# Optimization experiments

Hardware: AMD Instinct MI355X
Metric: run time of the kernel (lower is better)

The kernel has to match this reference:

```python
import jax, jax.numpy as jnp
import numpy as np

N_NODES = 50000
N_EDGES = 640000
D = 128
L = 3


def setup_inputs() -> dict:
    key = jax.random.key(0)
    k1, k2, k3, k4 = jax.random.split(key, 4)
    x = jax.random.normal(k1, (N_NODES, D), dtype=jnp.float32)
    # Glorot-ish scale so activations stay O(1) across 3 layers
    Ws = jax.random.normal(k2, (L, D, D), dtype=jnp.float32) * (1.0 / np.sqrt(D))
    bs = jnp.zeros((L, D), dtype=jnp.float32)
    edge_src = jax.random.randint(k3, (N_EDGES,), 0, N_NODES, dtype=jnp.int32)
    edge_dst = jax.random.randint(k4, (N_EDGES,), 0, N_NODES, dtype=jnp.int32)
    return {"x": x, "Ws": Ws, "bs": bs, "edge_src": edge_src, "edge_dst": edge_dst}


def reference(x, Ws, bs, edge_src, edge_dst):
    n = x.shape[0]
    ones = jnp.ones(edge_src.shape[0], dtype=x.dtype)
    # degrees, clamped to 1 as in dgl GraphConv(norm='both')
    deg_out = jnp.maximum(jax.ops.segment_sum(ones, edge_src, num_segments=n), 1.0)
    deg_in = jnp.maximum(jax.ops.segment_sum(ones, edge_dst, num_segments=n), 1.0)
    inv_sqrt_out = jax.lax.rsqrt(deg_out)[:, None]  # [N,1]
    inv_sqrt_in = jax.lax.rsqrt(deg_in)[:, None]    # [N,1]
    for l in range(Ws.shape[0]):
        h = x * inv_sqrt_out                         # src normalization
        msg = h[edge_src]                            # [E,D] gather
        agg = jax.ops.segment_sum(msg, edge_dst, num_segments=n)  # [N,D] scatter-add
        h = agg * inv_sqrt_in                        # dst normalization
        x = jax.nn.relu(h @ Ws[l] + bs[l])           # linear + ReLU
    return x
```

## Files before the change

kernel.cpp:

```cpp
#include <hip/hip_runtime.h>
#include <hip/hip_fp16.h>

typedef __attribute__((ext_vector_type(8))) _Float16 half8;
typedef __attribute__((ext_vector_type(4))) float f32x4;
typedef unsigned int u32;
typedef unsigned short u16;

#define ELL_PAD 64
#define NCHUNK 64
#define RSZ 8192


__global__ __launch_bounds__(256) void hist2(const int* __restrict__ esrc,
                                             const int* __restrict__ edst,
                                             u32* __restrict__ psrc,
                                             u32* __restrict__ pdst,
                                             const float* __restrict__ Ws,
                                             _Float16* __restrict__ Whi,
                                             _Float16* __restrict__ Wlo,
                                             int E, int N, int chunk, int R,
                                             int histBlocks, int packTotal) {
  __shared__ u32 bs_[RSZ];
  __shared__ u32 bd_[RSZ];
  if (blockIdx.x >= histBlocks) {
    int i = (blockIdx.x - histBlocks) * 256 + threadIdx.x;
    if (i < packTotal) {
      int lane  = i & 63;
      int kstep = (i >> 6) & 3;
      int ntile = (i >> 8) & 7;
      int layer = i >> 11;
      int n  = ntile * 16 + (lane & 15);
      int k0 = kstep * 32 + (lane >> 4) * 8;
      const float* W = Ws + (size_t)layer * 128 * 128;
      size_t base = (size_t)i * 8;
      for (int j = 0; j < 8; j++) {
        float v = W[(k0 + j) * 128 + n];
        _Float16 hi = (_Float16)v;
        Whi[base + j] = hi;
        Wlo[base + j] = (_Float16)(v - (float)hi);
      }
    }
    return;
  }
  int c = blockIdx.x / R;
  int r = blockIdx.x % R;
  int base = r * RSZ;
  int hi = min(RSZ, N - base);
  if (hi <= 0) return;
  for (int j = threadIdx.x; j < RSZ; j += 256) { bs_[j] = 0; bd_[j] = 0; }
  __syncthreads();
  int e0 = c * chunk;
  int e1 = min(E, e0 + chunk);
  for (int i = e0 + threadIdx.x; i < e1; i += 256) {
    unsigned ls = (unsigned)(esrc[i] - base);
    unsigned ld = (unsigned)(edst[i] - base);
    if (ls < (unsigned)RSZ) atomicAdd(&bs_[ls], 1u);
    if (ld < (unsigned)RSZ) atomicAdd(&bd_[ld], 1u);
  }
  __syncthreads();
  u32* ds = psrc + (size_t)c * N + base;
  u32* dd = pdst + (size_t)c * N + base;
  for (int j = threadIdx.x; j < hi; j += 256) { ds[j] = bs_[j]; dd[j] = bd_[j]; }
}


__global__ __launch_bounds__(256) void prep(const u32* __restrict__ psrc,
                                            u32* __restrict__ pdst,
                                            int* __restrict__ deg_out,
                                            int* __restrict__ deg_in, int N) {
  int i = blockIdx.x * 256 + threadIdx.x;
  if (i >= N) return;
  u32 s0 = 0, s1 = 0, s2 = 0, s3 = 0;
#pragma unroll
  for (int c = 0; c < NCHUNK; c += 4) {
    s0 += psrc[(size_t)(c + 0) * N + i];
    s1 += psrc[(size_t)(c + 1) * N + i];
    s2 += psrc[(size_t)(c + 2) * N + i];
    s3 += psrc[(size_t)(c + 3) * N + i];
  }
  deg_out[i] = (int)(s0 + s1 + s2 + s3);
  u32 cnt[NCHUNK];
#pragma unroll
  for (int c = 0; c < NCHUNK; c++) cnt[c] = pdst[(size_t)c * N + i];
  u32 run = (u32)i * ELL_PAD;
#pragma unroll
  for (int c = 0; c < NCHUNK; c++) { u32 t = cnt[c]; cnt[c] = run; run += t; }
#pragma unroll
  for (int c = 0; c < NCHUNK; c++) pdst[(size_t)c * N + i] = cnt[c];
  deg_in[i] = (int)(run - (u32)i * ELL_PAD);
}


__global__ __launch_bounds__(256) void xscale(const float* __restrict__ x,
                                              const int* __restrict__ deg_out,
                                              __half2* __restrict__ xh, int n64) {
  int gid = blockIdx.x * 256 + threadIdx.x;
  if (gid >= n64) return;
  int row = gid >> 6;
  int d = deg_out[row]; if (d < 1) d = 1;
  float s = rsqrtf((float)d);
  float2 v = ((const float2*)x)[gid];
  xh[gid] = __floats2half2_rn(v.x * s, v.y * s);
}


__global__ __launch_bounds__(256) void place(const int* __restrict__ esrc,
                                             const int* __restrict__ edst,
                                             const u32* __restrict__ pdst,
                                             u16* __restrict__ ell,
                                             int E, int N, int chunk, int R) {
  __shared__ u32 cur[RSZ];
  int c = blockIdx.x / R;
  int r = blockIdx.x % R;
  int base = r * RSZ;
  int hi = min(RSZ, N - base);
  if (hi <= 0) return;
  for (int j = threadIdx.x; j < hi; j += 256)
    cur[j] = pdst[(size_t)c * N + base + j];
  __syncthreads();
  int e0 = c * chunk;
  int e1 = min(E, e0 + chunk);
  for (int i = e0 + threadIdx.x; i < e1; i += 256) {
    int d = edst[i];
    unsigned loc = (unsigned)(d - base);
    if (loc < (unsigned)hi) {
      u32 p = atomicAdd(&cur[loc], 1u);
      u32 idx = p - (u32)d * ELL_PAD;
      if (idx < ELL_PAD) ell[p] = (u16)esrc[i];
    }
  }
}


__global__ __launch_bounds__(512) void layer16(const __half2* __restrict__ xh,
                                               const int* __restrict__ deg_in,
                                               const u16* __restrict__ ell,
                                               const _Float16* __restrict__ Whi,
                                               const _Float16* __restrict__ Wlo,
                                               const float* __restrict__ bias,
                                               const int* __restrict__ deg_out,
                                               __half* __restrict__ out16,
                                               float* __restrict__ out32, int n) {
  __shared__ _Float16 As[16 * 136];
  const int wave = threadIdx.x >> 6;
  const int lane = threadIdx.x & 63;
  const int rowBase = blockIdx.x * 16;

  {
    int r0 = rowBase + wave * 2, r1 = r0 + 1;
    int d0 = (r0 < n) ? deg_in[r0] : 0;
    int d1 = (r1 < n) ? deg_in[r1] : 0;
    int l0 = d0 > ELL_PAD ? ELL_PAD : d0;
    int l1 = d1 > ELL_PAD ? ELL_PAD : d1;
    const u16* ep0 = ell + (size_t)(r0 < n ? r0 : 0) * ELL_PAD;
    const u16* ep1 = ell + (size_t)(r1 < n ? r1 : 0) * ELL_PAD;
    float ax0 = 0.f, ay0 = 0.f, ax1 = 0.f, ay1 = 0.f;

    int m = (l0 < l1 ? l0 : l1) & ~3;
    int e = 0;
    for (; e < m; e += 4) {
      ushort4 ia = *(const ushort4*)&ep0[e];
      ushort4 ib = *(const ushort4*)&ep1[e];
      __half2 a0 = xh[(size_t)ia.x * 64 + lane];
      __half2 a1 = xh[(size_t)ia.y * 64 + lane];
      __half2 a2 = xh[(size_t)ia.z * 64 + lane];
      __half2 a3 = xh[(size_t)ia.w * 64 + lane];
      __half2 b0 = xh[(size_t)ib.x * 64 + lane];
      __half2 b1 = xh[(size_t)ib.y * 64 + lane];
      __half2 b2 = xh[(size_t)ib.z * 64 + lane];
      __half2 b3 = xh[(size_t)ib.w * 64 + lane];
      float2 u0 = __half22float2(a0), u1 = __half22float2(a1);
      float2 u2 = __half22float2(a2), u3 = __half22float2(a3);
      float2 w0 = __half22float2(b0), w1 = __half22float2(b1);
      float2 w2 = __half22float2(b2), w3 = __half22float2(b3);
      ax0 += (u0.x + u1.x) + (u2.x + u3.x);
      ay0 += (u0.y + u1.y) + (u2.y + u3.y);
      ax1 += (w0.x + w1.x) + (w2.x + w3.x);
      ay1 += (w0.y + w1.y) + (w2.y + w3.y);
    }
    int e0i = e;
    for (; e0i + 4 <= l0; e0i += 4) {
      ushort4 ia = *(const ushort4*)&ep0[e0i];
      __half2 a0 = xh[(size_t)ia.x * 64 + lane];
      __half2 a1 = xh[(size_t)ia.y * 64 + lane];
      __half2 a2 = xh[(size_t)ia.z * 64 + lane];
      __half2 a3 = xh[(size_t)ia.w * 64 + lane];
      float2 u0 = __half22float2(a0), u1 = __half22float2(a1);
      float2 u2 = __half22float2(a2), u3 = __half22float2(a3);
      ax0 += (u0.x + u1.x) + (u2.x + u3.x);
      ay0 += (u0.y + u1.y) + (u2.y + u3.y);
    }
    for (; e0i < l0; e0i++) {
      float2 v = __half22float2(xh[(size_t)ep0[e0i] * 64 + lane]);
      ax0 += v.x; ay0 += v.y;
    }
    int e1i = e;
    for (; e1i + 4 <= l1; e1i += 4) {
      ushort4 ib = *(const ushort4*)&ep1[e1i];
      __half2 b0 = xh[(size_t)ib.x * 64 + lane];
      __half2 b1 = xh[(size_t)ib.y * 64 + lane];
      __half2 b2 = xh[(size_t)ib.z * 64 + lane];
      __half2 b3 = xh[(size_t)ib.w * 64 + lane];
      float2 w0 = __half22float2(b0), w1 = __half22float2(b1);
      float2 w2 = __half22float2(b2), w3 = __half22float2(b3);
      ax1 += (w0.x + w1.x) + (w2.x + w3.x);
      ay1 += (w0.y + w1.y) + (w2.y + w3.y);
    }
    for (; e1i < l1; e1i++) {
      float2 v = __half22float2(xh[(size_t)ep1[e1i] * 64 + lane]);
      ax1 += v.x; ay1 += v.y;
    }

    float si0 = rsqrtf((float)(d0 < 1 ? 1 : d0));
    float si1 = rsqrtf((float)(d1 < 1 ? 1 : d1));
    *(__half2*)&As[(size_t)(wave * 2 + 0) * 136 + lane * 2] =
        __floats2half2_rn(ax0 * si0, ay0 * si0);
    *(__half2*)&As[(size_t)(wave * 2 + 1) * 136 + lane * 2] =
        __floats2half2_rn(ax1 * si1, ay1 * si1);
  }
  __syncthreads();

  const int quad = lane >> 4;
  const int l16  = lane & 15;
  f32x4 acc = (f32x4){0.f, 0.f, 0.f, 0.f};
#pragma unroll
  for (int ks = 0; ks < 4; ks++) {
    half8 a = *(const half8*)&As[(size_t)l16 * 136 + ks * 32 + quad * 8];
    half8 bh = *(const half8*)&Whi[((wave * 4 + ks) * 64 + lane) * 8];
    half8 bl = *(const half8*)&Wlo[((wave * 4 + ks) * 64 + lane) * 8];
    acc = __builtin_amdgcn_mfma_f32_16x16x32_f16(a, bh, acc, 0, 0, 0);
    acc = __builtin_amdgcn_mfma_f32_16x16x32_f16(a, bl, acc, 0, 0, 0);
  }

  const int r0 = rowBase + quad * 4;
  const int col = wave * 16 + l16;
  const float bv = bias[col];
#pragma unroll
  for (int r = 0; r < 4; r++) {
    int row = r0 + r;
    if (row < n) {
      float v = fmaxf(acc[r] + bv, 0.f);
      if (out16) {
        int d = deg_out[row]; if (d < 1) d = 1;
        out16[(size_t)row * 128 + col] = __float2half(v * rsqrtf((float)d));
      } else {
        out32[(size_t)row * 128 + col] = v;
      }
    }
  }
}


extern "C" void kernel_launch(void* const* d_in, const int* in_sizes, int n_in,
                              void* d_out, int out_size, void* d_ws, size_t ws_size,
                              hipStream_t stream) {
  const float* x   = (const float*)d_in[0];
  const float* Ws  = (const float*)d_in[1];
  const float* bs  = (const float*)d_in[2];
  const int* esrc  = (const int*)d_in[3];
  const int* edst  = (const int*)d_in[4];

  const int D = 128;
  const int N = in_sizes[0] / D;
  const int E = in_sizes[3];
  const int L = in_sizes[1] / (D * D);
  const int Npad = ((N + 15) / 16) * 16;
  const int chunk = (E + NCHUNK - 1) / NCHUNK;
  const int R = (N + RSZ - 1) / RSZ;
  const int histBlocks = NCHUNK * R;
  const int packTotal = L * 2048;
  const int packBlocks = (packTotal + 255) / 256;

  char* base = (char*)d_ws;
  size_t off = 0;
  auto alloc = [&](size_t bytes) {
    char* p = base + off;
    off = (off + bytes + 255) & ~(size_t)255;
    return p;
  };
  int*      deg_out = (int*)alloc((size_t)N * 4);
  int*      deg_in  = (int*)alloc((size_t)N * 4);
  u16*      ell     = (u16*)alloc((size_t)N * ELL_PAD * 2);
  _Float16* Whi     = (_Float16*)alloc((size_t)L * 16384 * 2);
  _Float16* Wlo     = (_Float16*)alloc((size_t)L * 16384 * 2);
  _Float16* xh0     = (_Float16*)alloc((size_t)Npad * 128 * 2);
  _Float16* xh1     = (_Float16*)alloc((size_t)Npad * 128 * 2);
  u32*      psrc    = (u32*)alloc((size_t)NCHUNK * N * 4);
  u32*      pdst    = (u32*)alloc((size_t)NCHUNK * N * 4);

  hist2<<<dim3(histBlocks + packBlocks), dim3(256), 0, stream>>>(
      esrc, edst, psrc, pdst, Ws, Whi, Wlo, E, N, chunk, R, histBlocks, packTotal);
  prep<<<dim3((N + 255) / 256), dim3(256), 0, stream>>>(psrc, pdst, deg_out, deg_in, N);
  xscale<<<dim3((N * 64 + 255) / 256), dim3(256), 0, stream>>>(
      x, deg_out, (__half2*)xh0, N * 64);
  place<<<dim3(histBlocks), dim3(256), 0, stream>>>(
      esrc, edst, pdst, ell, E, N, chunk, R);

  float* outf = (float*)d_out;
  _Float16* ping[2] = {xh0, xh1};
  const dim3 lgrid(Npad / 16), lblk(512);

  for (int l = 0; l < L; l++) {
    bool last = (l == L - 1);
    layer16<<<lgrid, lblk, 0, stream>>>(
        (const __half2*)ping[l & 1], deg_in, ell,
        Whi + (size_t)l * 16384, Wlo + (size_t)l * 16384,
        bs + (size_t)l * D, deg_out,
        last ? nullptr : (__half*)ping[(l + 1) & 1],
        last ? outf : nullptr, N);
  }
}
```

Before: 264.1 us.

## Build ELL with global atomics and gather four neighbors per wave with 16-byte loads

The chunked shared-memory histogram, prefix-scan and placement kernels are replaced by one edge-parallel kernel. It uses global atomics on the degree arrays to count degrees and place ELL entries directly, which drops the large per-chunk partial-count buffers and two launches. ELL rows are padded to a multiple of four with a dummy zero-filled node, so the aggregation loop needs no scalar tails. Each wave now splits into four 16-lane groups that each gather a different neighbor row with half8 loads, then combine the partial sums with cross-lane shuffles. In exchange, neighbor order within each ELL row becomes nondeterministic and the global atomics contend on high-degree nodes.

Result: no change. 262.6 us (-0.6%).

```diff
diff --git a/kernel.cpp b/kernel.cpp
--- a/kernel.cpp
+++ b/kernel.cpp
@@ -5,95 +5,69 @@
 typedef __attribute__((ext_vector_type(4))) float f32x4;
 typedef unsigned int u32;
 typedef unsigned short u16;
+typedef unsigned long long u64;
 
 #define ELL_PAD 64
-#define NCHUNK 64
-#define RSZ 8192
-
-
-__global__ __launch_bounds__(256) void hist2(const int* __restrict__ esrc,
+
+
+__global__ __launch_bounds__(256) void initpack(int* __restrict__ deg_out,
+                                                int* __restrict__ deg_in,
+                                                u32* __restrict__ xz0,
+                                                u32* __restrict__ xz1,
+                                                const float* __restrict__ Ws,
+                                                _Float16* __restrict__ Whi,
+                                                _Float16* __restrict__ Wlo,
+                                                int N, int padU32, int zb, int packTotal) {
+  int b = blockIdx.x;
+  if (b < zb) {
+    int i = b * 256 + threadIdx.x;
+    if (i < N) { deg_out[i] = 0; deg_in[i] = 0; }
+    if (b == 0) {
+      for (int j = threadIdx.x; j < padU32; j += 256) { xz0[j] = 0; xz1[j] = 0; }
+    }
+    return;
+  }
+  int i = (b - zb) * 256 + threadIdx.x;
+  if (i < packTotal) {
+    int lane  = i & 63;
+    int kstep = (i >> 6) & 3;
+    int ntile = (i >> 8) & 7;
+    int layer = i >> 11;
+    int nn = ntile * 16 + (lane & 15);
+    int k0 = kstep * 32 + (lane >> 4) * 8;
+    const float* W = Ws + (size_t)layer * 128 * 128;
+    size_t base = (size_t)i * 8;
+    for (int j = 0; j < 8; j++) {
+      float v = W[(k0 + j) * 128 + nn];
+      _Float16 hi = (_Float16)v;
+      Whi[base + j] = hi;
+      Wlo[base + j] = (_Float16)(v - (float)hi);
+    }
+  }
+}
+
+
+__global__ __launch_bounds__(256) void build(const int* __restrict__ esrc,
                                              const int* __restrict__ edst,
-                                             u32* __restrict__ psrc,
-                                             u32* __restrict__ pdst,
-                                             const float* __restrict__ Ws,
-                                             _Float16* __restrict__ Whi,
-                                             _Float16* __restrict__ Wlo,
-                                             int E, int N, int chunk, int R,
-                                             int histBlocks, int packTotal) {
-  __shared__ u32 bs_[RSZ];
-  __shared__ u32 bd_[RSZ];
-  if (blockIdx.x >= histBlocks) {
-    int i = (blockIdx.x - histBlocks) * 256 + threadIdx.x;
-    if (i < packTotal) {
-      int lane  = i & 63;
-      int kstep = (i >> 6) & 3;
-      int ntile = (i >> 8) & 7;
-      int layer = i >> 11;
-      int n  = ntile * 16 + (lane & 15);
-      int k0 = kstep * 32 + (lane >> 4) * 8;
-      const float* W = Ws + (size_t)layer * 128 * 128;
-      size_t base = (size_t)i * 8;
-      for (int j = 0; j < 8; j++) {
-        float v = W[(k0 + j) * 128 + n];
-        _Float16 hi = (_Float16)v;
-        Whi[base + j] = hi;
-        Wlo[base + j] = (_Float16)(v - (float)hi);
-      }
-    }
-    return;
-  }
-  int c = blockIdx.x / R;
-  int r = blockIdx.x % R;
-  int base = r * RSZ;
-  int hi = min(RSZ, N - base);
-  if (hi <= 0) return;
-  for (int j = threadIdx.x; j < RSZ; j += 256) { bs_[j] = 0; bd_[j] = 0; }
-  __syncthreads();
-  int e0 = c * chunk;
-  int e1 = min(E, e0 + chunk);
-  for (int i = e0 + threadIdx.x; i < e1; i += 256) {
-    unsigned ls = (unsigned)(esrc[i] - base);
-    unsigned ld = (unsigned)(edst[i] - base);
-    if (ls < (unsigned)RSZ) atomicAdd(&bs_[ls], 1u);
-    if (ld < (unsigned)RSZ) atomicAdd(&bd_[ld], 1u);
-  }
-  __syncthreads();
-  u32* ds = psrc + (size_t)c * N + base;
-  u32* dd = pdst + (size_t)c * N + base;
-  for (int j = threadIdx.x; j < hi; j += 256) { ds[j] = bs_[j]; dd[j] = bd_[j]; }
-}
-
-
-__global__ __launch_bounds__(256) void prep(const u32* __restrict__ psrc,
-                                            u32* __restrict__ pdst,
-                                            int* __restrict__ deg_out,
-                                            int* __restrict__ deg_in, int N) {
+                                             int* __restrict__ deg_out,
+                                             int* __restrict__ deg_in,
+                                             u16* __restrict__ ell, int E) {
   int i = blockIdx.x * 256 + threadIdx.x;
-  if (i >= N) return;
-  u32 s0 = 0, s1 = 0, s2 = 0, s3 = 0;
-#pragma unroll
-  for (int c = 0; c < NCHUNK; c += 4) {
-    s0 += psrc[(size_t)(c + 0) * N + i];
-    s1 += psrc[(size_t)(c + 1) * N + i];
-    s2 += psrc[(size_t)(c + 2) * N + i];
-    s3 += psrc[(size_t)(c + 3) * N + i];
-  }
-  deg_out[i] = (int)(s0 + s1 + s2 + s3);
-  u32 cnt[NCHUNK];
-#pragma unroll
-  for (int c = 0; c < NCHUNK; c++) cnt[c] = pdst[(size_t)c * N + i];
-  u32 run = (u32)i * ELL_PAD;
-#pragma unroll
-  for (int c = 0; c < NCHUNK; c++) { u32 t = cnt[c]; cnt[c] = run; run += t; }
-#pragma unroll
-  for (int c = 0; c < NCHUNK; c++) pdst[(size_t)c * N + i] = cnt[c];
-  deg_in[i] = (int)(run - (u32)i * ELL_PAD);
+  if (i >= E) return;
+  int s = esrc[i];
+  int d = edst[i];
+  atomicAdd(&deg_out[s], 1);
+  int p = atomicAdd(&deg_in[d], 1);
+  if (p < ELL_PAD) ell[(u32)d * ELL_PAD + (u32)p] = (u16)s;
 }
 
 
 __global__ __launch_bounds__(256) void xscale(const float* __restrict__ x,
                                               const int* __restrict__ deg_out,
-                                              __half2* __restrict__ xh, int n64) {
+                                              const int* __restrict__ deg_in,
+                                              __half2* __restrict__ xh,
+                                              u16* __restrict__ ell,
+                                              int N, int n64) {
   int gid = blockIdx.x * 256 + threadIdx.x;
   if (gid >= n64) return;
   int row = gid >> 6;
@@ -101,38 +75,17 @@
   float s = rsqrtf((float)d);
   float2 v = ((const float2*)x)[gid];
   xh[gid] = __floats2half2_rn(v.x * s, v.y * s);
-}
-
-
-__global__ __launch_bounds__(256) void place(const int* __restrict__ esrc,
-                                             const int* __restrict__ edst,
-                                             const u32* __restrict__ pdst,
-                                             u16* __restrict__ ell,
-                                             int E, int N, int chunk, int R) {
-  __shared__ u32 cur[RSZ];
-  int c = blockIdx.x / R;
-  int r = blockIdx.x % R;
-  int base = r * RSZ;
-  int hi = min(RSZ, N - base);
-  if (hi <= 0) return;
-  for (int j = threadIdx.x; j < hi; j += 256)
-    cur[j] = pdst[(size_t)c * N + base + j];
-  __syncthreads();
-  int e0 = c * chunk;
-  int e1 = min(E, e0 + chunk);
-  for (int i = e0 + threadIdx.x; i < e1; i += 256) {
-    int d = edst[i];
-    unsigned loc = (unsigned)(d - base);
-    if (loc < (unsigned)hi) {
-      u32 p = atomicAdd(&cur[loc], 1u);
-      u32 idx = p - (u32)d * ELL_PAD;
-      if (idx < ELL_PAD) ell[p] = (u16)esrc[i];
-    }
-  }
-}
-
-
-__global__ __launch_bounds__(512) void layer16(const __half2* __restrict__ xh,
+  if ((gid & 63) == 0) {
+    int c = deg_in[row];
+    int l = c > ELL_PAD ? ELL_PAD : c;
+    int t = (l + 3) & ~3;
+    u16* ep = ell + (u32)row * ELL_PAD;
+    for (int q = l; q < t; q++) ep[q] = (u16)N;
+  }
+}
+
+
+__global__ __launch_bounds__(512) void layer16(const _Float16* __restrict__ xh,
                                                const int* __restrict__ deg_in,
                                                const u16* __restrict__ ell,
                                                const _Float16* __restrict__ Whi,
@@ -144,7 +97,12 @@
   __shared__ _Float16 As[16 * 136];
   const int wave = threadIdx.x >> 6;
   const int lane = threadIdx.x & 63;
+  const int sub  = lane & 15;
+  const int grp  = lane >> 4;
+  const int sh   = grp << 4;
+  const u32 sub16 = (u32)sub * 16u;
   const int rowBase = blockIdx.x * 16;
+  const char* __restrict__ xb = (const char*)xh;
 
   {
     int r0 = rowBase + wave * 2, r1 = r0 + 1;
@@ -152,92 +110,99 @@
     int d1 = (r1 < n) ? deg_in[r1] : 0;
     int l0 = d0 > ELL_PAD ? ELL_PAD : d0;
     int l1 = d1 > ELL_PAD ? ELL_PAD : d1;
-    const u16* ep0 = ell + (size_t)(r0 < n ? r0 : 0) * ELL_PAD;
-    const u16* ep1 = ell + (size_t)(r1 < n ? r1 : 0) * ELL_PAD;
-    float ax0 = 0.f, ay0 = 0.f, ax1 = 0.f, ay1 = 0.f;
-
-    int m = (l0 < l1 ? l0 : l1) & ~3;
+    int t0 = (l0 + 3) & ~3;
+    int t1 = (l1 + 3) & ~3;
+    const u16* ep0 = ell + (u32)(r0 < n ? r0 : 0) * ELL_PAD;
+    const u16* ep1 = ell + (u32)(r1 < n ? r1 : 0) * ELL_PAD;
+
+    float a0[8] = {0.f, 0.f, 0.f, 0.f, 0.f, 0.f, 0.f, 0.f};
+    float a1[8] = {0.f, 0.f, 0.f, 0.f, 0.f, 0.f, 0.f, 0.f};
+
+    int m = t0 < t1 ? t0 : t1;
     int e = 0;
+    for (; e + 8 <= m; e += 8) {
+      u64 wa0 = *(const u64*)&ep0[e];
+      u64 wa1 = *(const u64*)&ep0[e + 4];
+      u64 wb0 = *(const u64*)&ep1[e];
+      u64 wb1 = *(const u64*)&ep1[e + 4];
+      u32 ia0 = ((u32)(wa0 >> sh) & 0xFFFFu) * 256u + sub16;
+      u32 ia1 = ((u32)(wa1 >> sh) & 0xFFFFu) * 256u + sub16;
+      u32 ib0 = ((u32)(wb0 >> sh) & 0xFFFFu) * 256u + sub16;
+      u32 ib1 = ((u32)(wb1 >> sh) & 0xFFFFu) * 256u + sub16;
+      half8 va0 = *(const half8*)(xb + ia0);
+      half8 va1 = *(const half8*)(xb + ia1);
+      half8 vb0 = *(const half8*)(xb + ib0);
+      half8 vb1 = *(const half8*)(xb + ib1);
+#pragma unroll
+      for (int j = 0; j < 8; j++) {
+        a0[j] += (float)va0[j] + (float)va1[j];
+        a1[j] += (float)vb0[j] + (float)vb1[j];
+      }
+    }
     for (; e < m; e += 4) {
-      ushort4 ia = *(const ushort4*)&ep0[e];
-      ushort4 ib = *(const ushort4*)&ep1[e];
-      __half2 a0 = xh[(size_t)ia.x * 64 + lane];
-      __half2 a1 = xh[(size_t)ia.y * 64 + lane];
-      __half2 a2 = xh[(size_t)ia.z * 64 + lane];
-      __half2 a3 = xh[(size_t)ia.w * 64 + lane];
-      __half2 b0 = xh[(size_t)ib.x * 64 + lane];
-      __half2 b1 = xh[(size_t)ib.y * 64 + lane];
-      __half2 b2 = xh[(size_t)ib.z * 64 + lane];
-      __half2 b3 = xh[(size_t)ib.w * 64 + lane];
-      float2 u0 = __half22float2(a0), u1 = __half22float2(a1);
-      float2 u2 = __half22float2(a2), u3 = __half22float2(a3);
-      float2 w0 = __half22float2(b0), w1 = __half22float2(b1);
-      float2 w2 = __half22float2(b2), w3 = __half22float2(b3);
-      ax0 += (u0.x + u1.x) + (u2.x + u3.x);
-      ay0 += (u0.y + u1.y) + (u2.y + u3.y);
-      ax1 += (w0.x + w1.x) + (w2.x + w3.x);
-      ay1 += (w0.y + w1.y) + (w2.y + w3.y);
-    }
-    int e0i = e;
-    for (; e0i + 4 <= l0; e0i += 4) {
-      ushort4 ia = *(const ushort4*)&ep0[e0i];
-      __half2 a0 = xh[(size_t)ia.x * 64 + lane];
-      __half2 a1 = xh[(size_t)ia.y * 64 + lane];
-      __half2 a2 = xh[(size_t)ia.z * 64 + lane];
-      __half2 a3 = xh[(size_t)ia.w * 64 + lane];
-      float2 u0 = __half22float2(a0), u1 = __half22float2(a1);
-      float2 u2 = __half22float2(a2), u3 = __half22float2(a3);
-      ax0 += (u0.x + u1.x) + (u2.x + u3.x);
-      ay0 += (u0.y + u1.y) + (u2.y + u3.y);
-    }
-    for (; e0i < l0; e0i++) {
-      float2 v = __half22float2(xh[(size_t)ep0[e0i] * 64 + lane]);
-      ax0 += v.x; ay0 += v.y;
-    }
-    int e1i = e;
-    for (; e1i + 4 <= l1; e1i += 4) {
-      ushort4 ib = *(const ushort4*)&ep1[e1i];
-      __half2 b0 = xh[(size_t)ib.x * 64 + lane];
-      __half2 b1 = xh[(size_t)ib.y * 64 + lane];
-      __half2 b2 = xh[(size_t)ib.z * 64 + lane];
-      __half2 b3 = xh[(size_t)ib.w * 64 + lane];
-      float2 w0 = __half22float2(b0), w1 = __half22float2(b1);
-      float2 w2 = __half22float2(b2), w3 = __half22float2(b3);
-      ax1 += (w0.x + w1.x) + (w2.x + w3.x);
-      ay1 += (w0.y + w1.y) + (w2.y + w3.y);
-    }
-    for (; e1i < l1; e1i++) {
-      float2 v = __half22float2(xh[(size_t)ep1[e1i] * 64 + lane]);
-      ax1 += v.x; ay1 += v.y;
+      u64 wa = *(const u64*)&ep0[e];
+      u64 wb = *(const u64*)&ep1[e];
+      u32 ia = ((u32)(wa >> sh) & 0xFFFFu) * 256u + sub16;
+      u32 ib = ((u32)(wb >> sh) & 0xFFFFu) * 256u + sub16;
+      half8 va = *(const half8*)(xb + ia);
+      half8 vb = *(const half8*)(xb + ib);
+#pragma unroll
+      for (int j = 0; j < 8; j++) { a0[j] += (float)va[j]; a1[j] += (float)vb[j]; }
+    }
+    for (int ea = m; ea < t0; ea += 4) {
+      u64 wa = *(const u64*)&ep0[ea];
+      u32 ia = ((u32)(wa >> sh) & 0xFFFFu) * 256u + sub16;
+      half8 va = *(const half8*)(xb + ia);
+#pragma unroll
+      for (int j = 0; j < 8; j++) a0[j] += (float)va[j];
+    }
+    for (int eb = m; eb < t1; eb += 4) {
+      u64 wb = *(const u64*)&ep1[eb];
+      u32 ib = ((u32)(wb >> sh) & 0xFFFFu) * 256u + sub16;
+      half8 vb = *(const half8*)(xb + ib);
+#pragma unroll
+      for (int j = 0; j < 8; j++) a1[j] += (float)vb[j];
+    }
+
+#pragma unroll
+    for (int j = 0; j < 8; j++) {
+      a0[j] += __shfl_xor(a0[j], 16, 64);
+      a0[j] += __shfl_xor(a0[j], 32, 64);
+      a1[j] += __shfl_xor(a1[j], 16, 64);
+      a1[j] += __shfl_xor(a1[j], 32, 64);
     }
 
     float si0 = rsqrtf((float)(d0 < 1 ? 1 : d0));
     float si1 = rsqrtf((float)(d1 < 1 ? 1 : d1));
-    *(__half2*)&As[(size_t)(wave * 2 + 0) * 136 + lane * 2] =
-        __floats2half2_rn(ax0 * si0, ay0 * si0);
-    *(__half2*)&As[(size_t)(wave * 2 + 1) * 136 + lane * 2] =
-        __floats2half2_rn(ax1 * si1, ay1 * si1);
+    if (grp == 0) {
+      half8 h0, h1;
+#pragma unroll
+      for (int j = 0; j < 8; j++) {
+        h0[j] = (_Float16)(a0[j] * si0);
+        h1[j] = (_Float16)(a1[j] * si1);
+      }
+      *(half8*)&As[(wave * 2 + 0) * 136 + sub * 8] = h0;
+      *(half8*)&As[(wave * 2 + 1) * 136 + sub * 8] = h1;
+    }
   }
   __syncthreads();
 
-  const int quad = lane >> 4;
-  const int l16  = lane & 15;
   f32x4 acc = (f32x4){0.f, 0.f, 0.f, 0.f};
 #pragma unroll
   for (int ks = 0; ks < 4; ks++) {
-    half8 a = *(const half8*)&As[(size_t)l16 * 136 + ks * 32 + quad * 8];
+    half8 a  = *(const half8*)&As[(size_t)sub * 136 + ks * 32 + grp * 8];
     half8 bh = *(const half8*)&Whi[((wave * 4 + ks) * 64 + lane) * 8];
     half8 bl = *(const half8*)&Wlo[((wave * 4 + ks) * 64 + lane) * 8];
     acc = __builtin_amdgcn_mfma_f32_16x16x32_f16(a, bh, acc, 0, 0, 0);
     acc = __builtin_amdgcn_mfma_f32_16x16x32_f16(a, bl, acc, 0, 0, 0);
   }
 
-  const int r0 = rowBase + quad * 4;
-  const int col = wave * 16 + l16;
+  const int r0c = rowBase + grp * 4;
+  const int col = wave * 16 + sub;
   const float bv = bias[col];
 #pragma unroll
   for (int r = 0; r < 4; r++) {
-    int row = r0 + r;
+    int row = r0c + r;
     if (row < n) {
       float v = fmaxf(acc[r] + bv, 0.f);
       if (out16) {
@@ -265,11 +230,6 @@
   const int E = in_sizes[3];
   const int L = in_sizes[1] / (D * D);
   const int Npad = ((N + 15) / 16) * 16;
-  const int chunk = (E + NCHUNK - 1) / NCHUNK;
-  const int R = (N + RSZ - 1) / RSZ;
-  const int histBlocks = NCHUNK * R;
-  const int packTotal = L * 2048;
-  const int packBlocks = (packTotal + 255) / 256;
 
   char* base = (char*)d_ws;
   size_t off = 0;
@@ -283,18 +243,22 @@
   u16*      ell     = (u16*)alloc((size_t)N * ELL_PAD * 2);
   _Float16* Whi     = (_Float16*)alloc((size_t)L * 16384 * 2);
   _Float16* Wlo     = (_Float16*)alloc((size_t)L * 16384 * 2);
-  _Float16* xh0     = (_Float16*)alloc((size_t)Npad * 128 * 2);
-  _Float16* xh1     = (_Float16*)alloc((size_t)Npad * 128 * 2);
-  u32*      psrc    = (u32*)alloc((size_t)NCHUNK * N * 4);
-  u32*      pdst    = (u32*)alloc((size_t)NCHUNK * N * 4);
-
-  hist2<<<dim3(histBlocks + packBlocks), dim3(256), 0, stream>>>(
-      esrc, edst, psrc, pdst, Ws, Whi, Wlo, E, N, chunk, R, histBlocks, packTotal);
-  prep<<<dim3((N + 255) / 256), dim3(256), 0, stream>>>(psrc, pdst, deg_out, deg_in, N);
+  _Float16* xh0     = (_Float16*)alloc((size_t)(Npad + 16) * 128 * 2);
+  _Float16* xh1     = (_Float16*)alloc((size_t)(Npad + 16) * 128 * 2);
+
+  const int zb = (N + 255) / 256;
+  const int packTotal = L * 2048;
+  const int packB = (packTotal + 255) / 256;
+  const int padU32 = 16 * 64;
+
+  initpack<<<dim3(zb + packB), dim3(256), 0, stream>>>(
+      deg_out, deg_in,
+      (u32*)(xh0 + (size_t)N * 128), (u32*)(xh1 + (size_t)N * 128),
+      Ws, Whi, Wlo, N, padU32, zb, packTotal);
+  build<<<dim3((E + 255) / 256), dim3(256), 0, stream>>>(
+      esrc, edst, deg_out, deg_in, ell, E);
   xscale<<<dim3((N * 64 + 255) / 256), dim3(256), 0, stream>>>(
-      x, deg_out, (__half2*)xh0, N * 64);
-  place<<<dim3(histBlocks), dim3(256), 0, stream>>>(
-      esrc, edst, pdst, ell, E, N, chunk, R);
+      x, deg_out, deg_in, (__half2*)xh0, ell, N, N * 64);
 
   float* outf = (float*)d_out;
   _Float16* ping[2] = {xh0, xh1};
@@ -303,7 +267,7 @@
   for (int l = 0; l < L; l++) {
     bool last = (l == L - 1);
     layer16<<<lgrid, lblk, 0, stream>>>(
-        (const __half2*)ping[l & 1], deg_in, ell,
+        (const _Float16*)ping[l & 1], deg_in, ell,
         Whi + (size_t)l * 16384, Wlo + (size_t)l * 16384,
         bs + (size_t)l * D, deg_out,
         last ? nullptr : (__half*)ping[(l + 1) & 1],
```
